# Optimization experiments

Hardware: AMD Instinct MI355X
Metric: run time of the kernel (lower is better)

## Reference

```python
import jax, jax.numpy as jnp
from jax import lax
import numpy as np

V, E, H, B, T = 512, 512, 1024, 128, 512

def _xavier(key, shape):
    fan_out, fan_in = shape
    bound = float(np.sqrt(6.0 / (fan_in + fan_out)))
    return jax.random.uniform(key, shape, jnp.float32, -bound, bound)

def setup_inputs() -> dict:
    key = jax.random.key(0)
    ks = jax.random.split(key, 6)
    src = jax.random.randint(ks[0], (B, T), 0, V, dtype=jnp.int32)
    embedding = _xavier(ks[1], (V, E))
    w_ih_l0 = _xavier(ks[2], (3 * H, E))
    w_hh_l0 = _xavier(ks[3], (3 * H, H))
    w_ih_l1 = _xavier(ks[4], (3 * H, H))
    w_hh_l1 = _xavier(ks[5], (3 * H, H))
    zb = jnp.zeros((3 * H,), jnp.float32)  # biases init'd to 0 in module
    return {
        "src": src, "embedding": embedding,
        "w_ih_l0": w_ih_l0, "w_hh_l0": w_hh_l0, "b_ih_l0": zb, "b_hh_l0": zb,
        "w_ih_l1": w_ih_l1, "w_hh_l1": w_hh_l1, "b_ih_l1": zb, "b_hh_l1": zb,
    }

def _gru_layer(x_seq, w_ih, w_hh, b_ih, b_hh):
    # x_seq: [B, T, D]. Precompute all input projections as one big GEMM.
    gates_x = jnp.einsum('btd,gd->btg', x_seq, w_ih) + b_ih  # [B, T, 3H]
    h_dim = w_hh.shape[1]
    w_hh_t = w_hh.T  # [H, 3H]

    def step(h, gx):
        gh = h @ w_hh_t + b_hh                      # [B, 3H]
        xr, xz, xn = jnp.split(gx, 3, axis=-1)
        hr, hz, hn = jnp.split(gh, 3, axis=-1)
        r = jax.nn.sigmoid(xr + hr)
        z = jax.nn.sigmoid(xz + hz)
        n = jnp.tanh(xn + r * hn)
        h_new = (1.0 - z) * n + z * h
        return h_new, h_new

    h0 = jnp.zeros((x_seq.shape[0], h_dim), x_seq.dtype)
    h_last, outs = lax.scan(step, h0, jnp.swapaxes(gates_x, 0, 1))  # time-major scan
    return jnp.swapaxes(outs, 0, 1), h_last  # [B, T, H], [B, H]

def reference(src, embedding, w_ih_l0, w_hh_l0, b_ih_l0, b_hh_l0,
              w_ih_l1, w_hh_l1, b_ih_l1, b_hh_l1):
    x = embedding[src]  # [B, T, E]
    y0, h0 = _gru_layer(x, w_ih_l0, w_hh_l0, b_ih_l0, b_hh_l0)
    _, h1 = _gru_layer(y0, w_ih_l1, w_hh_l1, b_ih_l1, b_hh_l1)
    return jnp.stack([h0, h1], axis=0)  # (n_layers, B, H)
```

## Files before the change

kernel.cpp:

```cpp
#include <hip/hip_runtime.h>
#include <type_traits>

typedef __attribute__((ext_vector_type(8))) short short8;
typedef __attribute__((ext_vector_type(4))) float f32x4;
typedef __attribute__((ext_vector_type(2))) unsigned long long u64x2;

constexpr int Bsz = 128;
constexpr int Tlen = 512;
constexpr int Hd = 1024;
constexpr int K1 = 2048;

__device__ __forceinline__ unsigned short f2b(float f) {
  unsigned int u = __float_as_uint(f);
  u = (u + 0x7FFFu + ((u >> 16) & 1u)) >> 16;
  return (unsigned short)u;
}
__device__ __forceinline__ unsigned long long aload64(const unsigned long long* p) {
  return __hip_atomic_load(p, __ATOMIC_RELAXED, __HIP_MEMORY_SCOPE_AGENT);
}
__device__ __forceinline__ unsigned int aload32(const unsigned int* p) {
  return __hip_atomic_load(p, __ATOMIC_RELAXED, __HIP_MEMORY_SCOPE_AGENT);
}
__device__ __forceinline__ void astore32(unsigned int* p, unsigned int v) {
  __hip_atomic_store(p, v, __ATOMIC_RELAXED, __HIP_MEMORY_SCOPE_AGENT);
}

template <int LAYER>
__device__ __forceinline__ void run_layer(
    const int* __restrict__ src, const float* __restrict__ P,
    const unsigned short* __restrict__ Wh, const unsigned short* __restrict__ Wx,
    const float* __restrict__ bhh, const float* __restrict__ bih,
    float* __restrict__ dout, unsigned short* __restrict__ Ab,
    unsigned short* __restrict__ A1,
    unsigned short* __restrict__ Stile,
    unsigned int* __restrict__ flags,
    unsigned int* __restrict__ lline,
    f32x4 (*__restrict__ red)[4][3][64],
    const int R0, const int J0, const int w, const int lane,
    const int m, const int tid)
{
  constexpr int KSZ = LAYER ? 2048 : 1024;
  constexpr int NKH = 8;
  constexpr int NKX = LAYER ? 8 : 0;
  constexpr int KE  = NKH + NKX;
  constexpr int PD  = 3;
  constexpr int PW  = 4;
  constexpr int NQ  = LAYER ? 4 : 3;
  constexpr int SLICE = KSZ / 8;
  constexpr int CPR   = SLICE / 8;
  constexpr int LG    = LAYER ? 5 : 4;
  constexpr int CH    = LAYER ? 8 : 4;

  const int lrow = lane >> 4;
  const int lcol = lane & 15;
  const int col = J0 + lcol;

  const float bhr = bhh[col], bhz = bhh[1024 + col], bhn = bhh[2048 + col];
  float gbr = 0.f, gbz = 0.f, gbn = 0.f;
  if (LAYER) { gbr = bih[col]; gbz = bih[1024 + col]; gbn = bih[2048 + col]; }

  short8 wBh[3][NKH];
#pragma unroll
  for (int g = 0; g < 3; ++g) {
    const unsigned short* wp = Wh + (g * 1024 + col) * 1024 + w * 256 + lrow * 8;
#pragma unroll
    for (int ks = 0; ks < NKH; ++ks)
      wBh[g][ks] = *(const short8*)(wp + ks * 32);
  }
  const unsigned short* wxp[3];
  if (LAYER) {
#pragma unroll
    for (int g = 0; g < 3; ++g)
      wxp[g] = Wx + (g * 1024 + col) * 1024 + w * 256 + lrow * 8;
  }

  const int myrow0 = R0 + w * 16 + lrow * 4;
  float hold[4] = {0.f, 0.f, 0.f, 0.f};

  for (int r = 0; r <= 512; ++r) {
    const bool active = LAYER ? (r >= 1) : (r < 512);
    if (active) {
      const bool first = LAYER ? (r == 1) : (r == 0);
      const int par = r & 1;
      const unsigned short* Acur = Ab + par * (Bsz * KSZ);
      unsigned short* Anext = Ab + (par ^ 1) * (Bsz * KSZ);
      const bool doGemm = !(LAYER == 0 && first);

      if (doGemm) {
#pragma unroll
        for (int s = 0; s < CH; ++s) {
          const int cid = tid + s * 256;
          const int row = cid >> LG;
          const int kk = m * SLICE + (cid & (CPR - 1)) * 8;
          if (!(LAYER && first && kk < 1024)) {
            const unsigned long long* ap = (const unsigned long long*)(
                Acur + (R0 + row) * KSZ + kk);
            u64x2 v;
            v[0] = aload64(ap);
            v[1] = aload64(ap + 1);
            *(u64x2*)(Stile + row * KSZ + kk) = v;
          }
        }
      }

      short8 wx[LAYER ? PW : 1][3];
      if (LAYER) {
#pragma unroll
        for (int j = 0; j < PW; ++j)
#pragma unroll
          for (int g = 0; g < 3; ++g)
            wx[j][g] = *(const short8*)(wxp[g] + j * 32);
      }

      float gpr[4], gpz[4], gpn[4];
      if (LAYER == 0) {
        int sv[4];
#pragma unroll
        for (int i = 0; i < 4; ++i) sv[i] = src[(myrow0 + i) * Tlen + r];
#pragma unroll
        for (int i = 0; i < 4; ++i) {
          const float* pr = P + sv[i] * 3072 + col;
          gpr[i] = pr[0]; gpz[i] = pr[1024]; gpn[i] = pr[2048];
        }
      } else {
#pragma unroll
        for (int i = 0; i < 4; ++i) { gpr[i] = gbr; gpz[i] = gbz; gpn[i] = gbn; }
      }

      if (doGemm) {
        __syncthreads();
        if (tid == 0) astore32(&lline[m], (unsigned)(r + 1));
        if (w == 0) {
          const unsigned tgt = (unsigned)(r + 1);
          for (;;) {
            const unsigned v = (lane < 8) ? aload32(&lline[lane]) : tgt;
            if (__all(v >= tgt)) break;
          }
        }
        __syncthreads();
        __builtin_amdgcn_fence(__ATOMIC_ACQUIRE, "workgroup");
      }

      f32x4 ar[4], az[4], anh[4], anx[4];
#pragma unroll
      for (int f = 0; f < 4; ++f) {
        ar[f]  = (f32x4){0.f, 0.f, 0.f, 0.f};
        az[f]  = (f32x4){0.f, 0.f, 0.f, 0.f};
        anh[f] = (f32x4){0.f, 0.f, 0.f, 0.f};
        anx[f] = (f32x4){0.f, 0.f, 0.f, 0.f};
      }

      const unsigned short* rowb[4];
#pragma unroll
      for (int f = 0; f < 4; ++f)
        rowb[f] = Stile + (f * 16 + lcol) * KSZ + w * 256 + lrow * 8;

      auto kloop = [&](auto kbv) {
        constexpr int kb = decltype(kbv)::value;
        short8 abuf[PD][4];
#pragma unroll
        for (int s = 0; s < PD; ++s) {
          const int ks = kb + s;
          if (ks < KE) {
#pragma unroll
            for (int f = 0; f < 4; ++f)
              abuf[s][f] = *(const short8*)(
                  rowb[f] + ks * 32 + ((LAYER && ks >= NKH) ? 768 : 0));
          }
        }
#pragma unroll
        for (int ks = kb; ks < KE; ++ks) {
          short8 br, bz, bn;
          if (ks < NKH) { br = wBh[0][ks]; bz = wBh[1][ks]; bn = wBh[2][ks]; }
          else {
            br = wx[(ks - NKH) % PW][0];
            bz = wx[(ks - NKH) % PW][1];
            bn = wx[(ks - NKH) % PW][2];
          }
#pragma unroll
          for (int f = 0; f < 4; ++f) {
            const short8 a = abuf[(ks - kb) % PD][f];
            ar[f] = __builtin_amdgcn_mfma_f32_16x16x32_bf16(a, br, ar[f], 0, 0, 0);
            az[f] = __builtin_amdgcn_mfma_f32_16x16x32_bf16(a, bz, az[f], 0, 0, 0);
            if (ks < NKH)
              anh[f] = __builtin_amdgcn_mfma_f32_16x16x32_bf16(a, bn, anh[f], 0, 0, 0);
            else
              anx[f] = __builtin_amdgcn_mfma_f32_16x16x32_bf16(a, bn, anx[f], 0, 0, 0);
          }
          const int kn = ks + PD;
          if (kn < KE) {
#pragma unroll
            for (int f = 0; f < 4; ++f)
              abuf[(ks - kb) % PD][f] = *(const short8*)(
                  rowb[f] + kn * 32 + ((LAYER && kn >= NKH) ? 768 : 0));
          }
          if (LAYER && ks >= NKH) {
            const int jn = (ks - NKH) + PW;
            if (jn < NKX) {
#pragma unroll
              for (int g = 0; g < 3; ++g)
                wx[(ks - NKH) % PW][g] = *(const short8*)(wxp[g] + jn * 32);
            }
          }
        }
      };
      if (doGemm) {
        if (!first) kloop(std::integral_constant<int, 0>{});
        else if (NKX > 0) kloop(std::integral_constant<int, NKH>{});
      }

#pragma unroll
      for (int f = 0; f < 4; ++f) {
        if (f != w) {
          const int sl = (f < w) ? f : f - 1;
          red[w][0][sl][lane] = ar[f];
          red[w][1][sl][lane] = az[f];
          red[w][2][sl][lane] = anh[f];
          if (NQ == 4) red[w][3][sl][lane] = anx[f];
        }
      }
      __syncthreads();
      f32x4 sr  = (f32x4){0.f, 0.f, 0.f, 0.f};
      f32x4 sz_ = (f32x4){0.f, 0.f, 0.f, 0.f};
      f32x4 snh = (f32x4){0.f, 0.f, 0.f, 0.f};
      f32x4 snx = (f32x4){0.f, 0.f, 0.f, 0.f};
#pragma unroll
      for (int f = 0; f < 4; ++f)
        if (f == w) { sr = ar[f]; sz_ = az[f]; snh = anh[f]; if (NQ == 4) snx = anx[f]; }
#pragma unroll
      for (int ww = 0; ww < 4; ++ww) {
        if (ww != w) {
          const int sl = (w < ww) ? w : w - 1;
          sr  += red[ww][0][sl][lane];
          sz_ += red[ww][1][sl][lane];
          snh += red[ww][2][sl][lane];
          if (NQ == 4) snx += red[ww][3][sl][lane];
        }
      }

      const bool lastw = LAYER ? (r == 512) : (r == 511);
#pragma unroll
      for (int i = 0; i < 4; ++i) {
        const int row = myrow0 + i;
        float rg = sr[i] + gpr[i] + bhr;
        rg = 1.f / (1.f + __expf(-rg));
        float zg = sz_[i] + gpz[i] + bhz;
        zg = 1.f / (1.f + __expf(-zg));
        const float nx = (snx[i] + gpn[i]) + rg * (snh[i] + bhn);
        const float e2 = __expf(2.f * fabsf(nx));
        const float ng = copysignf(1.f - 2.f / (e2 + 1.f), nx);
        const float hnew = (1.f - zg) * ng + zg * hold[i];
        hold[i] = hnew;
        const unsigned int hb = (unsigned int)f2b(hnew);
        const unsigned int nb = (unsigned int)__shfl_down((int)hb, 1, 64);
        if ((lcol & 1) == 0) {
          const unsigned int pv = hb | (nb << 16);
          astore32((unsigned int*)(Anext + row * KSZ + J0 + lcol), pv);
          if (LAYER == 0)
            astore32((unsigned int*)(A1 + (par ^ 1) * (Bsz * K1) +
                                     row * K1 + 1024 + J0 + lcol), pv);
        }
        if (lastw) dout[LAYER * (Bsz * Hd) + row * Hd + col] = hnew;
      }
    }

    if (r < 512) {
      __syncthreads();
      if (w == 0) {
        const unsigned tgt = (unsigned)(r + 1);
        if (lane == 0) astore32(&flags[(unsigned)blockIdx.x * 16u], tgt);
        for (;;) {
          const unsigned m0 = aload32(&flags[(unsigned)(lane)       * 16u]);
          const unsigned m1 = aload32(&flags[(unsigned)(lane + 64)  * 16u]);
          const unsigned m2 = aload32(&flags[(unsigned)(lane + 128) * 16u]);
          const unsigned m3 = aload32(&flags[(unsigned)(lane + 192) * 16u]);
          if (__all(m0 >= tgt && m1 >= tgt && m2 >= tgt && m3 >= tgt)) break;
          __builtin_amdgcn_s_sleep(1);
        }
      }
      __syncthreads();
    }
  }
}

__global__ void __launch_bounds__(256, 1) gru_persist(
    const int* __restrict__ src,
    const float* __restrict__ P,
    const unsigned short* __restrict__ Whh0b,
    const unsigned short* __restrict__ Whh1b,
    const unsigned short* __restrict__ Wih1b,
    const float* __restrict__ bhh0,
    const float* __restrict__ bih1,
    const float* __restrict__ bhh1,
    float* __restrict__ dout,
    unsigned short* __restrict__ A0,
    unsigned short* __restrict__ A1,
    unsigned short* __restrict__ Stage,
    unsigned int* __restrict__ flags,
    unsigned int* __restrict__ lflags,
    int* __restrict__ taken)
{
  __shared__ f32x4 red[4][4][3][64];
  __shared__ int s_work;

  const int tid = threadIdx.x;

  if (tid == 0) {
    unsigned int xcc;
    asm volatile("s_getreg_b32 %0, hwreg(HW_REG_XCC_ID)" : "=s"(xcc));
    const int pref = ((int)(xcc & 7u)) * 32;
    int got = -1;
    for (int j = 0; j < 256; ++j) {
      const int idx = (pref + j) & 255;
      int expected = 0;
      if (__hip_atomic_compare_exchange_strong(&taken[idx], &expected, 1,
              __ATOMIC_RELAXED, __ATOMIC_RELAXED, __HIP_MEMORY_SCOPE_AGENT)) {
        got = idx; break;
      }
    }
    s_work = got;
  }
  __syncthreads();
  const int work = s_work;
  const int xcd_w = work >> 5;
  const int slot = work & 31;
  const int layer = (slot >> 4) & 1;
  const int m = (slot >> 1) & 7;
  const int c = xcd_w * 8 + m;
  const int mh = slot & 1;
  const int R0 = mh * 64;
  const int J0 = c * 16;

  const int w = tid >> 6;
  const int lane = tid & 63;

  unsigned short* Stile = Stage + xcd_w * 393216 +
      (layer == 0 ? mh * 65536 : 131072 + mh * 131072);
  unsigned int* lline = lflags + (xcd_w * 4 + layer * 2 + mh) * 16;

  if (layer == 0)
    run_layer<0>(src, P, Whh0b, Wih1b, bhh0, bih1, dout, A0, A1, Stile,
                 flags, lline, red, R0, J0, w, lane, m, tid);
  else
    run_layer<1>(src, P, Whh1b, Wih1b, bhh1, bih1, dout, A1, A1, Stile,
                 flags, lline, red, R0, J0, w, lane, m, tid);
}

__global__ void __launch_bounds__(256) cvt_k(const float* __restrict__ s,
                                            unsigned short* __restrict__ d, int n) {
  const int i = (blockIdx.x * 256 + threadIdx.x) * 8;
  if (i >= n) return;
  const float4 a = *(const float4*)(s + i);
  const float4 b = *(const float4*)(s + i + 4);
  short8 o;
  o[0] = (short)f2b(a.x); o[1] = (short)f2b(a.y);
  o[2] = (short)f2b(a.z); o[3] = (short)f2b(a.w);
  o[4] = (short)f2b(b.x); o[5] = (short)f2b(b.y);
  o[6] = (short)f2b(b.z); o[7] = (short)f2b(b.w);
  *(short8*)(d + i) = o;
}

__global__ void __launch_bounds__(256) pemb_k(const float* __restrict__ emb,
                                             const float* __restrict__ wih0,
                                             const float* __restrict__ bih0,
                                             float* __restrict__ P) {
  __shared__ float se[64 * 64];
  const int g = blockIdx.x * 256 + threadIdx.x;
  const int v0 = blockIdx.y * 64;
  float acc[64];
#pragma unroll
  for (int i = 0; i < 64; ++i) acc[i] = 0.f;
  for (int kb = 0; kb < 8; ++kb) {
    __syncthreads();
#pragma unroll
    for (int s = 0; s < 4; ++s) {
      const int idx = threadIdx.x + s * 256;
      const int vv = idx >> 4, k4 = (idx & 15) * 4;
      *(float4*)(se + vv * 64 + k4) =
          *(const float4*)(emb + (v0 + vv) * 512 + kb * 64 + k4);
    }
    __syncthreads();
    float4 wv[16];
#pragma unroll
    for (int j = 0; j < 16; ++j)
      wv[j] = *(const float4*)(wih0 + g * 512 + kb * 64 + j * 4);
    for (int vv = 0; vv < 64; ++vv) {
      const float* er = se + vv * 64;
      float s0 = acc[vv];
#pragma unroll
      for (int j = 0; j < 16; ++j) {
        const float4 e = *(const float4*)(er + j * 4);
        s0 += wv[j].x * e.x + wv[j].y * e.y + wv[j].z * e.z + wv[j].w * e.w;
      }
      acc[vv] = s0;
    }
  }
  const float bb = bih0[g];
  for (int vv = 0; vv < 64; ++vv) P[(v0 + vv) * 3072 + g] = acc[vv] + bb;
}

__global__ void zero_k(unsigned int* flags, int* taken, unsigned int* lflags) {
  const int i = threadIdx.x;
  for (int j = 0; j < 16; ++j) flags[i * 16 + j] = 0u;
  taken[i] = 0;
  lflags[i] = 0u;
  lflags[i + 256] = 0u;
}

extern "C" void kernel_launch(void* const* d_in, const int* in_sizes, int n_in,
                              void* d_out, int out_size, void* d_ws, size_t ws_size,
                              hipStream_t stream) {
  const int* src = (const int*)d_in[0];
  const float* emb = (const float*)d_in[1];
  const float* wih0 = (const float*)d_in[2];
  const float* whh0 = (const float*)d_in[3];
  const float* bih0 = (const float*)d_in[4];
  const float* bhh0 = (const float*)d_in[5];
  const float* wih1 = (const float*)d_in[6];
  const float* whh1 = (const float*)d_in[7];
  const float* bih1 = (const float*)d_in[8];
  const float* bhh1 = (const float*)d_in[9];
  float* dout = (float*)d_out;

  char* p = (char*)d_ws;
  unsigned short* A0 = (unsigned short*)p;
  unsigned short* A1 = (unsigned short*)(p + 524288);
  unsigned short* Whh0b = (unsigned short*)(p + 1572864);
  unsigned short* Whh1b = (unsigned short*)(p + 7864320);
  unsigned short* Wih1b = (unsigned short*)(p + 14155776);
  float* P = (float*)(p + 20447232);
  unsigned int* flags = (unsigned int*)(p + 26738688);
  int* taken = (int*)(p + 26755072);
  unsigned int* lflags = (unsigned int*)(p + 26756096);
  unsigned short* Stage = (unsigned short*)(p + 26758144);

  constexpr int NW = 3072 * 1024;
  hipLaunchKernelGGL(cvt_k, dim3(NW / (256 * 8)), dim3(256), 0, stream, whh0, Whh0b, NW);
  hipLaunchKernelGGL(cvt_k, dim3(NW / (256 * 8)), dim3(256), 0, stream, whh1, Whh1b, NW);
  hipLaunchKernelGGL(cvt_k, dim3(NW / (256 * 8)), dim3(256), 0, stream, wih1, Wih1b, NW);
  hipLaunchKernelGGL(pemb_k, dim3(12, 8), dim3(256), 0, stream, emb, wih0, bih0, P);
  hipLaunchKernelGGL(zero_k, dim3(1), dim3(256), 0, stream, flags, taken, lflags);

  hipLaunchKernelGGL(gru_persist, dim3(256), dim3(256), 0, stream,
                     src, P, Whh0b, Whh1b, Wih1b, bhh0, bih1, bhh1,
                     dout, A0, A1, Stage, flags, lflags, taken);
}
```

Measured before the change: 8.659 ms.

## Replace global grid barrier with targeted producer flags and deeper buffering

The per-step all-block grid barrier is removed. Each block now publishes its own progress flag, and before staging a step it waits only on the specific producer blocks whose hidden-state slices it reads. The activation ring grows from 2 to 4 buffers and the LDS/staging tile is double-buffered, with a lagged global-minimum check to stop writers overwriting data that slow readers still need. The aim is to let blocks drift apart and cut barrier latency on the serial recurrence, at the cost of more workspace and more fragile producer/consumer indexing that could race if the pid mapping is wrong.

```diff
diff --git a/kernel.cpp b/kernel.cpp
--- a/kernel.cpp
+++ b/kernel.cpp
@@ -37,9 +37,11 @@
     unsigned int* __restrict__ lline,
     f32x4 (*__restrict__ red)[4][3][64],
     const int R0, const int J0, const int w, const int lane,
-    const int m, const int tid)
+    const int m, const int tid, const int work)
 {
   constexpr int KSZ = LAYER ? 2048 : 1024;
+  constexpr int RSZ = Bsz * KSZ;
+  constexpr int TILE = 64 * KSZ;
   constexpr int NKH = 8;
   constexpr int NKX = LAYER ? 8 : 0;
   constexpr int KE  = NKH + NKX;
@@ -54,6 +56,18 @@
   const int lrow = lane >> 4;
   const int lcol = lane & 15;
   const int col = J0 + lcol;
+  const int mh = R0 >> 6;
+
+  int pid = -1;
+  if (LAYER == 0) {
+    if (lane < 8) pid = m * 32 + lane * 2 + mh;
+  } else {
+    if (lane < 16) {
+      if (m < 4) pid = (2 * m + (lane >> 3)) * 32 + 16 + (lane & 7) * 2 + mh;
+      else       pid = (2 * (m - 4) + (lane >> 3)) * 32 + (lane & 7) * 2 + mh;
+    }
+  }
+  unsigned gmin = 0;
 
   const float bhr = bhh[col], bhz = bhh[1024 + col], bhn = bhh[2048 + col];
   float gbr = 0.f, gbz = 0.f, gbn = 0.f;
@@ -81,12 +95,45 @@
     const bool active = LAYER ? (r >= 1) : (r < 512);
     if (active) {
       const bool first = LAYER ? (r == 1) : (r == 0);
-      const int par = r & 1;
-      const unsigned short* Acur = Ab + par * (Bsz * KSZ);
-      unsigned short* Anext = Ab + (par ^ 1) * (Bsz * KSZ);
+      const unsigned short* Acur = Ab + (r & 3) * RSZ;
+      unsigned short* Anext = Ab + ((r + 1) & 3) * RSZ;
+      unsigned short* St = Stile + (r & 1) * TILE;
       const bool doGemm = !(LAYER == 0 && first);
 
+      short8 wx[LAYER ? PW : 1][3];
+      if (LAYER) {
+#pragma unroll
+        for (int j = 0; j < PW; ++j)
+#pragma unroll
+          for (int g = 0; g < 3; ++g)
+            wx[j][g] = *(const short8*)(wxp[g] + j * 32);
+      }
+      float gpr[4], gpz[4], gpn[4];
+      if (LAYER == 0) {
+        int sv[4];
+#pragma unroll
+        for (int i = 0; i < 4; ++i) sv[i] = src[(myrow0 + i) * Tlen + r];
+#pragma unroll
+        for (int i = 0; i < 4; ++i) {
+          const float* pr = P + sv[i] * 3072 + col;
+          gpr[i] = pr[0]; gpz[i] = pr[1024]; gpn[i] = pr[2048];
+        }
+      } else {
+#pragma unroll
+        for (int i = 0; i < 4; ++i) { gpr[i] = gbr; gpz[i] = gbz; gpn[i] = gbn; }
+      }
+
       if (doGemm) {
+        if (w == 0) {
+          const unsigned tgt = (unsigned)r;
+          for (;;) {
+            const unsigned v = (pid >= 0) ? aload32(&flags[pid]) : tgt;
+            if (__all(v >= tgt)) break;
+            __builtin_amdgcn_s_sleep(1);
+          }
+        }
+        __syncthreads();
+
 #pragma unroll
         for (int s = 0; s < CH; ++s) {
           const int cid = tid + s * 256;
@@ -98,36 +145,10 @@
             u64x2 v;
             v[0] = aload64(ap);
             v[1] = aload64(ap + 1);
-            *(u64x2*)(Stile + row * KSZ + kk) = v;
-          }
-        }
-      }
-
-      short8 wx[LAYER ? PW : 1][3];
-      if (LAYER) {
-#pragma unroll
-        for (int j = 0; j < PW; ++j)
-#pragma unroll
-          for (int g = 0; g < 3; ++g)
-            wx[j][g] = *(const short8*)(wxp[g] + j * 32);
-      }
-
-      float gpr[4], gpz[4], gpn[4];
-      if (LAYER == 0) {
-        int sv[4];
-#pragma unroll
-        for (int i = 0; i < 4; ++i) sv[i] = src[(myrow0 + i) * Tlen + r];
-#pragma unroll
-        for (int i = 0; i < 4; ++i) {
-          const float* pr = P + sv[i] * 3072 + col;
-          gpr[i] = pr[0]; gpz[i] = pr[1024]; gpn[i] = pr[2048];
-        }
-      } else {
-#pragma unroll
-        for (int i = 0; i < 4; ++i) { gpr[i] = gbr; gpz[i] = gbz; gpn[i] = gbn; }
-      }
-
-      if (doGemm) {
+            *(u64x2*)(St + row * KSZ + kk) = v;
+          }
+        }
+
         __syncthreads();
         if (tid == 0) astore32(&lline[m], (unsigned)(r + 1));
         if (w == 0) {
@@ -138,7 +159,7 @@
           }
         }
         __syncthreads();
-        __builtin_amdgcn_fence(__ATOMIC_ACQUIRE, "workgroup");
+        asm volatile("buffer_inv sc0" ::: "memory");
       }
 
       f32x4 ar[4], az[4], anh[4], anx[4];
@@ -153,7 +174,7 @@
       const unsigned short* rowb[4];
 #pragma unroll
       for (int f = 0; f < 4; ++f)
-        rowb[f] = Stile + (f * 16 + lcol) * KSZ + w * 256 + lrow * 8;
+        rowb[f] = St + (f * 16 + lcol) * KSZ + w * 256 + lrow * 8;
 
       auto kloop = [&](auto kbv) {
         constexpr int kb = decltype(kbv)::value;
@@ -217,6 +238,21 @@
           red[w][1][sl][lane] = az[f];
           red[w][2][sl][lane] = anh[f];
           if (NQ == 4) red[w][3][sl][lane] = anx[f];
+        }
+      }
+      if (w == 0 && r >= 3) {
+        const unsigned tgt = (unsigned)(r - 2);
+        if (gmin < tgt) {
+          for (;;) {
+            const unsigned a = aload32(&flags[lane]);
+            const unsigned b = aload32(&flags[lane + 64]);
+            const unsigned c2 = aload32(&flags[lane + 128]);
+            const unsigned d = aload32(&flags[lane + 192]);
+            if (__all(a >= tgt && b >= tgt && c2 >= tgt && d >= tgt)) {
+              gmin = tgt; break;
+            }
+            __builtin_amdgcn_s_sleep(1);
+          }
         }
       }
       __syncthreads();
@@ -257,28 +293,16 @@
           const unsigned int pv = hb | (nb << 16);
           astore32((unsigned int*)(Anext + row * KSZ + J0 + lcol), pv);
           if (LAYER == 0)
-            astore32((unsigned int*)(A1 + (par ^ 1) * (Bsz * K1) +
+            astore32((unsigned int*)(A1 + ((r + 1) & 3) * (Bsz * K1) +
                                      row * K1 + 1024 + J0 + lcol), pv);
         }
         if (lastw) dout[LAYER * (Bsz * Hd) + row * Hd + col] = hnew;
       }
-    }
-
-    if (r < 512) {
+
       __syncthreads();
-      if (w == 0) {
-        const unsigned tgt = (unsigned)(r + 1);
-        if (lane == 0) astore32(&flags[(unsigned)blockIdx.x * 16u], tgt);
-        for (;;) {
-          const unsigned m0 = aload32(&flags[(unsigned)(lane)       * 16u]);
-          const unsigned m1 = aload32(&flags[(unsigned)(lane + 64)  * 16u]);
-          const unsigned m2 = aload32(&flags[(unsigned)(lane + 128) * 16u]);
-          const unsigned m3 = aload32(&flags[(unsigned)(lane + 192) * 16u]);
-          if (__all(m0 >= tgt && m1 >= tgt && m2 >= tgt && m3 >= tgt)) break;
-          __builtin_amdgcn_s_sleep(1);
-        }
-      }
-      __syncthreads();
+      if (w == 0 && lane == 0) astore32(&flags[work], (unsigned)(r + 1));
+    } else {
+      if (w == 0 && lane == 0) astore32(&flags[work], (unsigned)(r + 1));
     }
   }
 }
@@ -334,16 +358,16 @@
   const int w = tid >> 6;
   const int lane = tid & 63;
 
-  unsigned short* Stile = Stage + xcd_w * 393216 +
-      (layer == 0 ? mh * 65536 : 131072 + mh * 131072);
+  unsigned short* Stile = Stage + xcd_w * 786432 +
+      (layer == 0 ? mh * 131072 : 262144 + mh * 262144);
   unsigned int* lline = lflags + (xcd_w * 4 + layer * 2 + mh) * 16;
 
   if (layer == 0)
     run_layer<0>(src, P, Whh0b, Wih1b, bhh0, bih1, dout, A0, A1, Stile,
-                 flags, lline, red, R0, J0, w, lane, m, tid);
+                 flags, lline, red, R0, J0, w, lane, m, tid, work);
   else
     run_layer<1>(src, P, Whh1b, Wih1b, bhh1, bih1, dout, A1, A1, Stile,
-                 flags, lline, red, R0, J0, w, lane, m, tid);
+                 flags, lline, red, R0, J0, w, lane, m, tid, work);
 }
 
 __global__ void __launch_bounds__(256) cvt_k(const float* __restrict__ s,
@@ -401,7 +425,7 @@
 
 __global__ void zero_k(unsigned int* flags, int* taken, unsigned int* lflags) {
   const int i = threadIdx.x;
-  for (int j = 0; j < 16; ++j) flags[i * 16 + j] = 0u;
+  flags[i] = 0u;
   taken[i] = 0;
   lflags[i] = 0u;
   lflags[i + 256] = 0u;
@@ -424,15 +448,15 @@
 
   char* p = (char*)d_ws;
   unsigned short* A0 = (unsigned short*)p;
-  unsigned short* A1 = (unsigned short*)(p + 524288);
-  unsigned short* Whh0b = (unsigned short*)(p + 1572864);
-  unsigned short* Whh1b = (unsigned short*)(p + 7864320);
-  unsigned short* Wih1b = (unsigned short*)(p + 14155776);
-  float* P = (float*)(p + 20447232);
-  unsigned int* flags = (unsigned int*)(p + 26738688);
-  int* taken = (int*)(p + 26755072);
-  unsigned int* lflags = (unsigned int*)(p + 26756096);
-  unsigned short* Stage = (unsigned short*)(p + 26758144);
+  unsigned short* A1 = (unsigned short*)(p + 1048576);
+  unsigned short* Whh0b = (unsigned short*)(p + 3145728);
+  unsigned short* Whh1b = (unsigned short*)(p + 9437184);
+  unsigned short* Wih1b = (unsigned short*)(p + 15728640);
+  float* P = (float*)(p + 22020096);
+  unsigned int* flags = (unsigned int*)(p + 28311552);
+  int* taken = (int*)(p + 28327936);
+  unsigned int* lflags = (unsigned int*)(p + 28328960);
+  unsigned short* Stage = (unsigned short*)(p + 28331008);
 
   constexpr int NW = 3072 * 1024;
   hipLaunchKernelGGL(cvt_k, dim3(NW / (256 * 8)), dim3(256), 0, stream, whh0, Whh0b, NW);
```

New measurement: 10.43 ms. +20.4%, slower.

## Replace flat grid barrier with hierarchical per-XCD aggregated barrier

Applied to the files above, without the earlier changes.

The per-step global barrier, where every block polled all 256 flags, becomes two levels. Per XCD and per row half, one aggregator block (the layer-0, m=0 one) waits for the 16 relevant block flags and then publishes an xflag. All blocks then poll only the 8 xflags for their row half. This cuts polling traffic and atomic contention on the flags. Separately, the workgroup acquire fence after the local barrier is replaced with an explicit buffer_inv sc0 cache invalidate. The trade-offs are an extra dependency hop through the aggregator and correctness that relies on the memory-scope assumptions behind that invalidate.

```diff
diff --git a/kernel.cpp b/kernel.cpp
--- a/kernel.cpp
+++ b/kernel.cpp
@@ -34,10 +34,11 @@
     unsigned short* __restrict__ A1,
     unsigned short* __restrict__ Stile,
     unsigned int* __restrict__ flags,
+    unsigned int* __restrict__ xflags,
     unsigned int* __restrict__ lline,
     f32x4 (*__restrict__ red)[4][3][64],
     const int R0, const int J0, const int w, const int lane,
-    const int m, const int tid)
+    const int m, const int tid, const int work, const int xcd_w)
 {
   constexpr int KSZ = LAYER ? 2048 : 1024;
   constexpr int NKH = 8;
@@ -54,6 +55,8 @@
   const int lrow = lane >> 4;
   const int lcol = lane & 15;
   const int col = J0 + lcol;
+  const int mh = R0 >> 6;
+  const bool isagg = (LAYER == 0) && (m == 0);
 
   const float bhr = bhh[col], bhz = bhh[1024 + col], bhn = bhh[2048 + col];
   float gbr = 0.f, gbz = 0.f, gbn = 0.f;
@@ -138,7 +141,7 @@
           }
         }
         __syncthreads();
-        __builtin_amdgcn_fence(__ATOMIC_ACQUIRE, "workgroup");
+        asm volatile("buffer_inv sc0" ::: "memory");
       }
 
       f32x4 ar[4], az[4], anh[4], anx[4];
@@ -268,14 +271,21 @@
       __syncthreads();
       if (w == 0) {
         const unsigned tgt = (unsigned)(r + 1);
-        if (lane == 0) astore32(&flags[(unsigned)blockIdx.x * 16u], tgt);
+        if (lane == 0) astore32(&flags[(unsigned)work * 16u], tgt);
+        if (isagg) {
+          const unsigned fid = (unsigned)(xcd_w * 32 + (int)lane * 2 + mh) * 16u;
+          for (;;) {
+            const unsigned v = (lane < 16) ? aload32(&flags[fid]) : tgt;
+            if (__all(v >= tgt)) break;
+            __builtin_amdgcn_s_sleep(2);
+          }
+          if (lane == 0) astore32(&xflags[(unsigned)(xcd_w * 2 + mh) * 16u], tgt);
+        }
+        const unsigned xid = (unsigned)((int)lane * 2 + mh) * 16u;
         for (;;) {
-          const unsigned m0 = aload32(&flags[(unsigned)(lane)       * 16u]);
-          const unsigned m1 = aload32(&flags[(unsigned)(lane + 64)  * 16u]);
-          const unsigned m2 = aload32(&flags[(unsigned)(lane + 128) * 16u]);
-          const unsigned m3 = aload32(&flags[(unsigned)(lane + 192) * 16u]);
-          if (__all(m0 >= tgt && m1 >= tgt && m2 >= tgt && m3 >= tgt)) break;
-          __builtin_amdgcn_s_sleep(1);
+          const unsigned v = (lane < 8) ? aload32(&xflags[xid]) : tgt;
+          if (__all(v >= tgt)) break;
+          __builtin_amdgcn_s_sleep(2);
         }
       }
       __syncthreads();
@@ -297,6 +307,7 @@
     unsigned short* __restrict__ A1,
     unsigned short* __restrict__ Stage,
     unsigned int* __restrict__ flags,
+    unsigned int* __restrict__ xflags,
     unsigned int* __restrict__ lflags,
     int* __restrict__ taken)
 {
@@ -340,10 +351,10 @@
 
   if (layer == 0)
     run_layer<0>(src, P, Whh0b, Wih1b, bhh0, bih1, dout, A0, A1, Stile,
-                 flags, lline, red, R0, J0, w, lane, m, tid);
+                 flags, xflags, lline, red, R0, J0, w, lane, m, tid, work, xcd_w);
   else
     run_layer<1>(src, P, Whh1b, Wih1b, bhh1, bih1, dout, A1, A1, Stile,
-                 flags, lline, red, R0, J0, w, lane, m, tid);
+                 flags, xflags, lline, red, R0, J0, w, lane, m, tid, work, xcd_w);
 }
 
 __global__ void __launch_bounds__(256) cvt_k(const float* __restrict__ s,
@@ -399,12 +410,14 @@
   for (int vv = 0; vv < 64; ++vv) P[(v0 + vv) * 3072 + g] = acc[vv] + bb;
 }
 
-__global__ void zero_k(unsigned int* flags, int* taken, unsigned int* lflags) {
+__global__ void zero_k(unsigned int* flags, int* taken, unsigned int* lflags,
+                       unsigned int* xflags) {
   const int i = threadIdx.x;
   for (int j = 0; j < 16; ++j) flags[i * 16 + j] = 0u;
   taken[i] = 0;
   lflags[i] = 0u;
   lflags[i + 256] = 0u;
+  xflags[i] = 0u;
 }
 
 extern "C" void kernel_launch(void* const* d_in, const int* in_sizes, int n_in,
@@ -432,16 +445,17 @@
   unsigned int* flags = (unsigned int*)(p + 26738688);
   int* taken = (int*)(p + 26755072);
   unsigned int* lflags = (unsigned int*)(p + 26756096);
-  unsigned short* Stage = (unsigned short*)(p + 26758144);
+  unsigned int* xflags = (unsigned int*)(p + 26758144);
+  unsigned short* Stage = (unsigned short*)(p + 26759168);
 
   constexpr int NW = 3072 * 1024;
   hipLaunchKernelGGL(cvt_k, dim3(NW / (256 * 8)), dim3(256), 0, stream, whh0, Whh0b, NW);
   hipLaunchKernelGGL(cvt_k, dim3(NW / (256 * 8)), dim3(256), 0, stream, whh1, Whh1b, NW);
   hipLaunchKernelGGL(cvt_k, dim3(NW / (256 * 8)), dim3(256), 0, stream, wih1, Wih1b, NW);
   hipLaunchKernelGGL(pemb_k, dim3(12, 8), dim3(256), 0, stream, emb, wih0, bih0, P);
-  hipLaunchKernelGGL(zero_k, dim3(1), dim3(256), 0, stream, flags, taken, lflags);
+  hipLaunchKernelGGL(zero_k, dim3(1), dim3(256), 0, stream, flags, taken, lflags, xflags);
 
   hipLaunchKernelGGL(gru_persist, dim3(256), dim3(256), 0, stream,
                      src, P, Whh0b, Whh1b, Wih1b, bhh0, bih1, bhh1,
-                     dout, A0, A1, Stage, flags, lflags, taken);
-}
+                     dout, A0, A1, Stage, flags, xflags, lflags, taken);
+}
```

New measurement: 8.685 ms. No clear change (+0.3%).

## Replace global grid barrier with per-domain dataflow flags and 8-slot ring buffers

Applied to the files above, without the earlier changes.

Removes the per-step all-block grid barrier and has each wave publish a per-domain progress flag after writing its hidden-state slice. Consumers wait only on the flags of the domain they read from. Hidden states go to 8-deep ring buffers (A0, A1h, A1x), and layer 1 splits its GEMM into an input part (from layer 0) and a recurrent part so the two layers can pipeline. A periodic back-pressure wait keeps producers from overrunning the ring. The cost is more flag polling and larger workspace, plus correctness risk in the ordering logic.

```diff
diff --git a/kernel.cpp b/kernel.cpp
--- a/kernel.cpp
+++ b/kernel.cpp
@@ -1,5 +1,4 @@
 #include <hip/hip_runtime.h>
-#include <type_traits>
 
 typedef __attribute__((ext_vector_type(8))) short short8;
 typedef __attribute__((ext_vector_type(4))) float f32x4;
@@ -8,7 +7,8 @@
 constexpr int Bsz = 128;
 constexpr int Tlen = 512;
 constexpr int Hd = 1024;
-constexpr int K1 = 2048;
+constexpr int RS = 128 * 1024;
+constexpr int NS = 8;
 
 __device__ __forceinline__ unsigned short f2b(float f) {
   unsigned int u = __float_as_uint(f);
@@ -30,41 +30,38 @@
     const int* __restrict__ src, const float* __restrict__ P,
     const unsigned short* __restrict__ Wh, const unsigned short* __restrict__ Wx,
     const float* __restrict__ bhh, const float* __restrict__ bih,
-    float* __restrict__ dout, unsigned short* __restrict__ Ab,
-    unsigned short* __restrict__ A1,
-    unsigned short* __restrict__ Stile,
+    float* __restrict__ dout,
+    unsigned short* __restrict__ A0,
+    unsigned short* __restrict__ A1h,
+    unsigned short* __restrict__ A1x,
+    unsigned short* __restrict__ stg0,
+    unsigned short* __restrict__ stgH,
     unsigned int* __restrict__ flags,
     unsigned int* __restrict__ lline,
     f32x4 (*__restrict__ red)[4][3][64],
     const int R0, const int J0, const int w, const int lane,
     const int m, const int tid)
 {
-  constexpr int KSZ = LAYER ? 2048 : 1024;
-  constexpr int NKH = 8;
-  constexpr int NKX = LAYER ? 8 : 0;
-  constexpr int KE  = NKH + NKX;
-  constexpr int PD  = 3;
-  constexpr int PW  = 4;
-  constexpr int NQ  = LAYER ? 4 : 3;
-  constexpr int SLICE = KSZ / 8;
-  constexpr int CPR   = SLICE / 8;
-  constexpr int LG    = LAYER ? 5 : 4;
-  constexpr int CH    = LAYER ? 8 : 4;
-
+  constexpr int PD = 3;
+  constexpr int NQ = LAYER ? 4 : 3;
   const int lrow = lane >> 4;
   const int lcol = lane & 15;
   const int col = J0 + lcol;
+  const int mh = R0 >> 6;
+  const int domL0 = mh;
+  const int domSelf = LAYER * 2 + mh;
+  const int c = J0 >> 4;
 
   const float bhr = bhh[col], bhz = bhh[1024 + col], bhn = bhh[2048 + col];
   float gbr = 0.f, gbz = 0.f, gbn = 0.f;
   if (LAYER) { gbr = bih[col]; gbz = bih[1024 + col]; gbn = bih[2048 + col]; }
 
-  short8 wBh[3][NKH];
+  short8 wBh[3][8];
 #pragma unroll
   for (int g = 0; g < 3; ++g) {
     const unsigned short* wp = Wh + (g * 1024 + col) * 1024 + w * 256 + lrow * 8;
 #pragma unroll
-    for (int ks = 0; ks < NKH; ++ks)
+    for (int ks = 0; ks < 8; ++ks)
       wBh[g][ks] = *(const short8*)(wp + ks * 32);
   }
   const unsigned short* wxp[3];
@@ -78,69 +75,11 @@
   float hold[4] = {0.f, 0.f, 0.f, 0.f};
 
   for (int r = 0; r <= 512; ++r) {
-    const bool active = LAYER ? (r >= 1) : (r < 512);
+    if (LAYER == 0 && r == 512) break;
+    const bool active = LAYER ? (r >= 1) : true;
+    const int scur = r & 7, snext = (r + 1) & 7;
+
     if (active) {
-      const bool first = LAYER ? (r == 1) : (r == 0);
-      const int par = r & 1;
-      const unsigned short* Acur = Ab + par * (Bsz * KSZ);
-      unsigned short* Anext = Ab + (par ^ 1) * (Bsz * KSZ);
-      const bool doGemm = !(LAYER == 0 && first);
-
-      if (doGemm) {
-#pragma unroll
-        for (int s = 0; s < CH; ++s) {
-          const int cid = tid + s * 256;
-          const int row = cid >> LG;
-          const int kk = m * SLICE + (cid & (CPR - 1)) * 8;
-          if (!(LAYER && first && kk < 1024)) {
-            const unsigned long long* ap = (const unsigned long long*)(
-                Acur + (R0 + row) * KSZ + kk);
-            u64x2 v;
-            v[0] = aload64(ap);
-            v[1] = aload64(ap + 1);
-            *(u64x2*)(Stile + row * KSZ + kk) = v;
-          }
-        }
-      }
-
-      short8 wx[LAYER ? PW : 1][3];
-      if (LAYER) {
-#pragma unroll
-        for (int j = 0; j < PW; ++j)
-#pragma unroll
-          for (int g = 0; g < 3; ++g)
-            wx[j][g] = *(const short8*)(wxp[g] + j * 32);
-      }
-
-      float gpr[4], gpz[4], gpn[4];
-      if (LAYER == 0) {
-        int sv[4];
-#pragma unroll
-        for (int i = 0; i < 4; ++i) sv[i] = src[(myrow0 + i) * Tlen + r];
-#pragma unroll
-        for (int i = 0; i < 4; ++i) {
-          const float* pr = P + sv[i] * 3072 + col;
-          gpr[i] = pr[0]; gpz[i] = pr[1024]; gpn[i] = pr[2048];
-        }
-      } else {
-#pragma unroll
-        for (int i = 0; i < 4; ++i) { gpr[i] = gbr; gpz[i] = gbz; gpn[i] = gbn; }
-      }
-
-      if (doGemm) {
-        __syncthreads();
-        if (tid == 0) astore32(&lline[m], (unsigned)(r + 1));
-        if (w == 0) {
-          const unsigned tgt = (unsigned)(r + 1);
-          for (;;) {
-            const unsigned v = (lane < 8) ? aload32(&lline[lane]) : tgt;
-            if (__all(v >= tgt)) break;
-          }
-        }
-        __syncthreads();
-        __builtin_amdgcn_fence(__ATOMIC_ACQUIRE, "workgroup");
-      }
-
       f32x4 ar[4], az[4], anh[4], anx[4];
 #pragma unroll
       for (int f = 0; f < 4; ++f) {
@@ -149,64 +88,144 @@
         anh[f] = (f32x4){0.f, 0.f, 0.f, 0.f};
         anx[f] = (f32x4){0.f, 0.f, 0.f, 0.f};
       }
-
-      const unsigned short* rowb[4];
-#pragma unroll
-      for (int f = 0; f < 4; ++f)
-        rowb[f] = Stile + (f * 16 + lcol) * KSZ + w * 256 + lrow * 8;
-
-      auto kloop = [&](auto kbv) {
-        constexpr int kb = decltype(kbv)::value;
+      float gpr[4], gpz[4], gpn[4];
+      if (LAYER == 0) {
+        int sv[4];
+#pragma unroll
+        for (int i = 0; i < 4; ++i) sv[i] = src[(myrow0 + i) * Tlen + r];
+#pragma unroll
+        for (int i = 0; i < 4; ++i) {
+          const float* pr = P + sv[i] * 3072 + col;
+          gpr[i] = pr[0]; gpz[i] = pr[1024]; gpn[i] = pr[2048];
+        }
+      } else {
+#pragma unroll
+        for (int i = 0; i < 4; ++i) { gpr[i] = gbr; gpz[i] = gbz; gpn[i] = gbn; }
+      }
+
+      unsigned short* s0 = stg0 + (r & 1) * 65536;
+      unsigned short* sH = stgH + (r & 1) * 65536;
+
+      auto detect = [&](int dom, unsigned tgt) {
+        if (w == 0) {
+          const unsigned int* fb = flags + dom * 256 + lane;
+          for (;;) {
+            const unsigned a = aload32(fb),        b = aload32(fb + 64),
+                           c2 = aload32(fb + 128), d = aload32(fb + 192);
+            if (__all(a >= tgt && b >= tgt && c2 >= tgt && d >= tgt)) break;
+            __builtin_amdgcn_s_sleep(1);
+          }
+        }
+        __syncthreads();
+      };
+      auto pullT = [&](const unsigned short* ring, unsigned short* stg) {
+#pragma unroll
+        for (int s = 0; s < 4; ++s) {
+          const int cid = tid + s * 256;
+          const int row = cid >> 4;
+          const int kk = m * 128 + (cid & 15) * 8;
+          const unsigned long long* ap = (const unsigned long long*)(
+              ring + (R0 + row) * 1024 + kk);
+          u64x2 v;
+          v[0] = aload64(ap);
+          v[1] = aload64(ap + 1);
+          *(u64x2*)(stg + row * 1024 + kk) = v;
+        }
+      };
+      auto localbar = [&](unsigned tgt) {
+        __syncthreads();
+        if (tid == 0) astore32(&lline[m], tgt);
+        if (w == 0) {
+          for (;;) {
+            const unsigned v = (lane < 8) ? aload32(&lline[lane]) : tgt;
+            if (__all(v >= tgt)) break;
+          }
+        }
+        __syncthreads();
+        asm volatile("buffer_inv sc0" ::: "memory");
+      };
+      auto gemm8 = [&](const unsigned short* stg, const short8 (&wB)[3][8],
+                       f32x4 (&a0)[4], f32x4 (&a1)[4], f32x4 (&a2)[4]) {
+        const unsigned short* rb[4];
+#pragma unroll
+        for (int f = 0; f < 4; ++f)
+          rb[f] = stg + (f * 16 + lcol) * 1024 + w * 256 + lrow * 8;
         short8 abuf[PD][4];
 #pragma unroll
-        for (int s = 0; s < PD; ++s) {
-          const int ks = kb + s;
-          if (ks < KE) {
+        for (int s = 0; s < PD; ++s)
+#pragma unroll
+          for (int f = 0; f < 4; ++f)
+            abuf[s][f] = *(const short8*)(rb[f] + s * 32);
+#pragma unroll
+        for (int ks = 0; ks < 8; ++ks) {
+#pragma unroll
+          for (int f = 0; f < 4; ++f) {
+            const short8 a = abuf[ks % PD][f];
+            a0[f] = __builtin_amdgcn_mfma_f32_16x16x32_bf16(a, wB[0][ks], a0[f], 0, 0, 0);
+            a1[f] = __builtin_amdgcn_mfma_f32_16x16x32_bf16(a, wB[1][ks], a1[f], 0, 0, 0);
+            a2[f] = __builtin_amdgcn_mfma_f32_16x16x32_bf16(a, wB[2][ks], a2[f], 0, 0, 0);
+          }
+          if (ks + PD < 8)
 #pragma unroll
             for (int f = 0; f < 4; ++f)
-              abuf[s][f] = *(const short8*)(
-                  rowb[f] + ks * 32 + ((LAYER && ks >= NKH) ? 768 : 0));
-          }
-        }
-#pragma unroll
-        for (int ks = kb; ks < KE; ++ks) {
-          short8 br, bz, bn;
-          if (ks < NKH) { br = wBh[0][ks]; bz = wBh[1][ks]; bn = wBh[2][ks]; }
-          else {
-            br = wx[(ks - NKH) % PW][0];
-            bz = wx[(ks - NKH) % PW][1];
-            bn = wx[(ks - NKH) % PW][2];
-          }
-#pragma unroll
-          for (int f = 0; f < 4; ++f) {
-            const short8 a = abuf[(ks - kb) % PD][f];
-            ar[f] = __builtin_amdgcn_mfma_f32_16x16x32_bf16(a, br, ar[f], 0, 0, 0);
-            az[f] = __builtin_amdgcn_mfma_f32_16x16x32_bf16(a, bz, az[f], 0, 0, 0);
-            if (ks < NKH)
-              anh[f] = __builtin_amdgcn_mfma_f32_16x16x32_bf16(a, bn, anh[f], 0, 0, 0);
-            else
+              abuf[ks % PD][f] = *(const short8*)(rb[f] + (ks + PD) * 32);
+        }
+      };
+
+      if (LAYER == 0) {
+        if (r > 0) {
+          detect(domL0, (unsigned)r);
+          pullT(A0 + scur * RS, s0);
+          localbar((unsigned)(r + 1));
+          gemm8(s0, wBh, ar, az, anh);
+        }
+      } else {
+        detect(domL0, (unsigned)r);
+        pullT(A1x + scur * RS, s0);
+        localbar((unsigned)(2 * r));
+        {
+          const unsigned short* rb[4];
+#pragma unroll
+          for (int f = 0; f < 4; ++f)
+            rb[f] = s0 + (f * 16 + lcol) * 1024 + w * 256 + lrow * 8;
+          short8 abuf[PD][4];
+#pragma unroll
+          for (int s = 0; s < PD; ++s)
+#pragma unroll
+            for (int f = 0; f < 4; ++f)
+              abuf[s][f] = *(const short8*)(rb[f] + s * 32);
+          short8 wxb[4][3];
+#pragma unroll
+          for (int j = 0; j < 4; ++j)
+#pragma unroll
+            for (int g = 0; g < 3; ++g)
+              wxb[j][g] = *(const short8*)(wxp[g] + j * 32);
+#pragma unroll
+          for (int ks = 0; ks < 8; ++ks) {
+            const short8 br = wxb[ks % 4][0], bz = wxb[ks % 4][1], bn = wxb[ks % 4][2];
+#pragma unroll
+            for (int f = 0; f < 4; ++f) {
+              const short8 a = abuf[ks % PD][f];
+              ar[f]  = __builtin_amdgcn_mfma_f32_16x16x32_bf16(a, br, ar[f], 0, 0, 0);
+              az[f]  = __builtin_amdgcn_mfma_f32_16x16x32_bf16(a, bz, az[f], 0, 0, 0);
               anx[f] = __builtin_amdgcn_mfma_f32_16x16x32_bf16(a, bn, anx[f], 0, 0, 0);
-          }
-          const int kn = ks + PD;
-          if (kn < KE) {
-#pragma unroll
-            for (int f = 0; f < 4; ++f)
-              abuf[(ks - kb) % PD][f] = *(const short8*)(
-                  rowb[f] + kn * 32 + ((LAYER && kn >= NKH) ? 768 : 0));
-          }
-          if (LAYER && ks >= NKH) {
-            const int jn = (ks - NKH) + PW;
-            if (jn < NKX) {
+            }
+            if (ks + PD < 8)
+#pragma unroll
+              for (int f = 0; f < 4; ++f)
+                abuf[ks % PD][f] = *(const short8*)(rb[f] + (ks + PD) * 32);
+            if (ks + 4 < 8)
 #pragma unroll
               for (int g = 0; g < 3; ++g)
-                wx[(ks - NKH) % PW][g] = *(const short8*)(wxp[g] + jn * 32);
-            }
-          }
-        }
-      };
-      if (doGemm) {
-        if (!first) kloop(std::integral_constant<int, 0>{});
-        else if (NKX > 0) kloop(std::integral_constant<int, NKH>{});
+                wxb[ks % 4][g] = *(const short8*)(wxp[g] + (ks + 4) * 32);
+          }
+        }
+        if (r > 1) {
+          detect(domSelf, (unsigned)r);
+          pullT(A1h + scur * RS, sH);
+          localbar((unsigned)(2 * r + 1));
+          gemm8(sH, wBh, ar, az, anh);
+        }
       }
 
 #pragma unroll
@@ -217,6 +236,23 @@
           red[w][1][sl][lane] = az[f];
           red[w][2][sl][lane] = anh[f];
           if (NQ == 4) red[w][3][sl][lane] = anx[f];
+        }
+      }
+      if (w == 0 && (r & 3) == 0 && r >= 8) {
+        const unsigned tgt = (unsigned)(r - 3);
+        const unsigned int* f1 = flags + (2 + mh) * 256 + lane;
+        const unsigned int* f0 = flags + mh * 256 + lane;
+        for (;;) {
+          unsigned a = aload32(f1), b = aload32(f1 + 64),
+                   c2 = aload32(f1 + 128), d = aload32(f1 + 192);
+          bool ok = a >= tgt && b >= tgt && c2 >= tgt && d >= tgt;
+          if (LAYER == 0) {
+            unsigned e = aload32(f0), f = aload32(f0 + 64),
+                     g = aload32(f0 + 128), h = aload32(f0 + 192);
+            ok = ok && e >= tgt && f >= tgt && g >= tgt && h >= tgt;
+          }
+          if (__all(ok)) break;
+          __builtin_amdgcn_s_sleep(1);
         }
       }
       __syncthreads();
@@ -255,31 +291,20 @@
         const unsigned int nb = (unsigned int)__shfl_down((int)hb, 1, 64);
         if ((lcol & 1) == 0) {
           const unsigned int pv = hb | (nb << 16);
-          astore32((unsigned int*)(Anext + row * KSZ + J0 + lcol), pv);
-          if (LAYER == 0)
-            astore32((unsigned int*)(A1 + (par ^ 1) * (Bsz * K1) +
-                                     row * K1 + 1024 + J0 + lcol), pv);
+          if (LAYER == 0) {
+            astore32((unsigned int*)(A0 + snext * RS + row * 1024 + J0 + lcol), pv);
+            astore32((unsigned int*)(A1x + snext * RS + row * 1024 + J0 + lcol), pv);
+          } else {
+            astore32((unsigned int*)(A1h + snext * RS + row * 1024 + J0 + lcol), pv);
+          }
         }
         if (lastw) dout[LAYER * (Bsz * Hd) + row * Hd + col] = hnew;
       }
     }
 
-    if (r < 512) {
-      __syncthreads();
-      if (w == 0) {
-        const unsigned tgt = (unsigned)(r + 1);
-        if (lane == 0) astore32(&flags[(unsigned)blockIdx.x * 16u], tgt);
-        for (;;) {
-          const unsigned m0 = aload32(&flags[(unsigned)(lane)       * 16u]);
-          const unsigned m1 = aload32(&flags[(unsigned)(lane + 64)  * 16u]);
-          const unsigned m2 = aload32(&flags[(unsigned)(lane + 128) * 16u]);
-          const unsigned m3 = aload32(&flags[(unsigned)(lane + 192) * 16u]);
-          if (__all(m0 >= tgt && m1 >= tgt && m2 >= tgt && m3 >= tgt)) break;
-          __builtin_amdgcn_s_sleep(1);
-        }
-      }
-      __syncthreads();
-    }
+    asm volatile("s_waitcnt vmcnt(0)" ::: "memory");
+    if (lane == 0)
+      astore32(&flags[domSelf * 256 + c * 4 + w], (unsigned)(r + 1));
   }
 }
 
@@ -294,7 +319,8 @@
     const float* __restrict__ bhh1,
     float* __restrict__ dout,
     unsigned short* __restrict__ A0,
-    unsigned short* __restrict__ A1,
+    unsigned short* __restrict__ A1h,
+    unsigned short* __restrict__ A1x,
     unsigned short* __restrict__ Stage,
     unsigned int* __restrict__ flags,
     unsigned int* __restrict__ lflags,
@@ -334,16 +360,17 @@
   const int w = tid >> 6;
   const int lane = tid & 63;
 
-  unsigned short* Stile = Stage + xcd_w * 393216 +
-      (layer == 0 ? mh * 65536 : 131072 + mh * 131072);
+  unsigned short* base = Stage + xcd_w * 786432;
+  unsigned short* stg0 = base + (layer ? 262144 : 0) + mh * 131072;
+  unsigned short* stgH = base + 524288 + mh * 131072;
   unsigned int* lline = lflags + (xcd_w * 4 + layer * 2 + mh) * 16;
 
   if (layer == 0)
-    run_layer<0>(src, P, Whh0b, Wih1b, bhh0, bih1, dout, A0, A1, Stile,
-                 flags, lline, red, R0, J0, w, lane, m, tid);
+    run_layer<0>(src, P, Whh0b, Wih1b, bhh0, bih1, dout, A0, A1h, A1x,
+                 stg0, stgH, flags, lline, red, R0, J0, w, lane, m, tid);
   else
-    run_layer<1>(src, P, Whh1b, Wih1b, bhh1, bih1, dout, A1, A1, Stile,
-                 flags, lline, red, R0, J0, w, lane, m, tid);
+    run_layer<1>(src, P, Whh1b, Wih1b, bhh1, bih1, dout, A0, A1h, A1x,
+                 stg0, stgH, flags, lline, red, R0, J0, w, lane, m, tid);
 }
 
 __global__ void __launch_bounds__(256) cvt_k(const float* __restrict__ s,
@@ -401,7 +428,7 @@
 
 __global__ void zero_k(unsigned int* flags, int* taken, unsigned int* lflags) {
   const int i = threadIdx.x;
-  for (int j = 0; j < 16; ++j) flags[i * 16 + j] = 0u;
+  flags[i] = 0u; flags[i + 256] = 0u; flags[i + 512] = 0u; flags[i + 768] = 0u;
   taken[i] = 0;
   lflags[i] = 0u;
   lflags[i + 256] = 0u;
@@ -423,16 +450,17 @@
   float* dout = (float*)d_out;
 
   char* p = (char*)d_ws;
-  unsigned short* A0 = (unsigned short*)p;
-  unsigned short* A1 = (unsigned short*)(p + 524288);
-  unsigned short* Whh0b = (unsigned short*)(p + 1572864);
-  unsigned short* Whh1b = (unsigned short*)(p + 7864320);
-  unsigned short* Wih1b = (unsigned short*)(p + 14155776);
-  float* P = (float*)(p + 20447232);
-  unsigned int* flags = (unsigned int*)(p + 26738688);
-  int* taken = (int*)(p + 26755072);
-  unsigned int* lflags = (unsigned int*)(p + 26756096);
-  unsigned short* Stage = (unsigned short*)(p + 26758144);
+  unsigned short* A0    = (unsigned short*)p;
+  unsigned short* A1h   = (unsigned short*)(p + 2097152);
+  unsigned short* A1x   = (unsigned short*)(p + 4194304);
+  unsigned short* Whh0b = (unsigned short*)(p + 6291456);
+  unsigned short* Whh1b = (unsigned short*)(p + 12582912);
+  unsigned short* Wih1b = (unsigned short*)(p + 18874368);
+  float* P              = (float*)(p + 25165824);
+  unsigned int* flags   = (unsigned int*)(p + 31457280);
+  unsigned int* lflags  = (unsigned int*)(p + 31461376);
+  int* taken            = (int*)(p + 31463424);
+  unsigned short* Stage = (unsigned short*)(p + 31464448);
 
   constexpr int NW = 3072 * 1024;
   hipLaunchKernelGGL(cvt_k, dim3(NW / (256 * 8)), dim3(256), 0, stream, whh0, Whh0b, NW);
@@ -443,5 +471,5 @@
 
   hipLaunchKernelGGL(gru_persist, dim3(256), dim3(256), 0, stream,
                      src, P, Whh0b, Whh1b, Wih1b, bhh0, bih1, bhh1,
-                     dout, A0, A1, Stage, flags, lflags, taken);
-}
+                     dout, A0, A1h, A1x, Stage, flags, lflags, taken);
+}
```

Result: slower. 10.98 ms (+26.8%).
